# Optimization experiments

Measured on AMD Instinct MI355X. Metric: run time of the kernel, lower is better.

The kernel has to match this reference:

```python
import jax, jax.numpy as jnp
import numpy as np

N, E, C_IN, C_OUT, HEADS = 50000, 800000, 256, 64, 4

def setup_inputs() -> dict:
    key = jax.random.key(0)
    ks = jax.random.split(key, 6)
    x = jax.random.normal(ks[0], (N, C_IN), dtype=jnp.float32)
    row = jax.random.randint(ks[1], (E,), 0, N, dtype=jnp.int32)
    col = jax.random.randint(ks[2], (E,), 0, N, dtype=jnp.int32)
    # ensure no self loops (remove_self_loops is then a no-op)
    col = jnp.where(col == row, (col + 1) % N, col)
    edge_index = jnp.stack([row, col], axis=0)
    edge_attr = jax.random.normal(ks[3], (E,), dtype=jnp.float32)
    weight = jax.random.normal(ks[4], (C_IN, C_OUT), dtype=jnp.float32) * (1.0 / np.sqrt(C_IN))
    kw, kb = jax.random.split(ks[5])
    att_w = jax.random.normal(kw, (2 * C_OUT, HEADS), dtype=jnp.float32) * (1.0 / np.sqrt(2 * C_OUT))
    att_b = jax.random.normal(kb, (HEADS,), dtype=jnp.float32) * 0.01
    return {"x": x, "edge_index": edge_index, "edge_attr": edge_attr,
            "weight": weight, "att_w": att_w, "att_b": att_b}

def _egat_forward(x, edge_index, edge_attr, weight, att_w, att_b):
    n = x.shape[0]
    xp = x @ weight  # [N, C_OUT]
    # add self loops (edge_attr fill value = 1)
    loop = jnp.arange(n, dtype=edge_index.dtype)
    row = jnp.concatenate([edge_index[0], loop])
    col = jnp.concatenate([edge_index[1], loop])
    ea = jnp.concatenate([edge_attr, jnp.ones((n,), dtype=edge_attr.dtype)])
    # per-edge attention logits [E+N, HEADS]
    alpha = jnp.concatenate([xp[row], xp[col]], axis=-1) @ att_w + att_b
    alpha = alpha * jnp.abs(ea)[:, None]
    alpha = jax.nn.leaky_relu(alpha, negative_slope=0.2) * 100.0
    # segment softmax grouped by row
    amax = jax.ops.segment_max(alpha, row, num_segments=n)
    ex = jnp.exp(alpha - amax[row])
    denom = jax.ops.segment_sum(ex, row, num_segments=n)
    alpha = ex / (denom[row] + 1e-16)
    # concat=False -> average heads into a single column
    alpha = alpha.mean(-1)[:, None]  # [E+N, 1]
    # my_cast: [E+N, C_OUT, n_cols]
    out = xp[col][:, :, None] * alpha[:, None, :]
    out = jax.ops.segment_sum(out, row, num_segments=n)  # [N, C_OUT, 1]
    alpha_index = jnp.stack([row, col], axis=0)
    return out, alpha, alpha_index

def reference(x, edge_index, edge_attr, weight, att_w, att_b):
    return _egat_forward(x, edge_index, edge_attr, weight, att_w, att_b)
```

## Files before the change

### kernel.cpp

```cpp
#include <hip/hip_runtime.h>
#include <hip/hip_bf16.h>

#define NN 50000
#define NE 800000
#define MT (NN + NE)
#define CO 64

#define OFF_ALPHA (NN * CO)
#define OFF_IDX   (OFF_ALPHA + MT)

#define WS_XPB  0
#define WS_A1   (WS_XPB + NN * CO / 2)
#define WS_A2   (WS_A1 + NN * 4)
#define WS_CNT  (WS_A2 + NN * 4)
#define WS_SLOT 2050000
#define WS_NEED4 ((size_t)14850000 * 4)

#define GEMM_BLOCKS ((NN + 63) / 64)
#define HIST_BLOCKS ((MT + 255) / 256)

template <bool S4>
__global__ __launch_bounds__(256) void k_gemm_hist(const float* __restrict__ x,
                                                   const float* __restrict__ w,
                                                   __hip_bfloat16* __restrict__ xpb,
                                                   const float* __restrict__ attw,
                                                   float* __restrict__ a1,
                                                   float* __restrict__ a2,
                                                   const int* __restrict__ ei0,
                                                   const int* __restrict__ ei1,
                                                   const float* __restrict__ ea,
                                                   int* __restrict__ cnt,
                                                   int* __restrict__ slot1,
                                                   int4* __restrict__ slot4,
                                                   float* __restrict__ dout) {
  if (blockIdx.x < GEMM_BLOCKS) {
    __shared__ float xs[32][68];
    __shared__ float wsm[32][68];
    const int tid = threadIdx.x;
    const int nb = blockIdx.x * 64;
    const int tr = tid >> 4;
    const int tc = tid & 15;
    const int xn0 = tid >> 3, xq0 = tid & 7;
    const int xn1 = (256 + tid) >> 3, xq1 = tid & 7;
    const int wk0 = tid >> 4, wc0 = tid & 15;
    const int wk1 = (256 + tid) >> 4, wc1 = tid & 15;
    float acc[4][4] = {};
    float4 xv0, xv1, wv0, wv1;

    {
      int gn0 = nb + xn0, gn1 = nb + xn1;
      xv0 = (gn0 < NN) ? *reinterpret_cast<const float4*>(&x[gn0 * 256 + xq0 * 4])
                       : make_float4(0.f, 0.f, 0.f, 0.f);
      xv1 = (gn1 < NN) ? *reinterpret_cast<const float4*>(&x[gn1 * 256 + xq1 * 4])
                       : make_float4(0.f, 0.f, 0.f, 0.f);
      wv0 = *reinterpret_cast<const float4*>(&w[wk0 * CO + wc0 * 4]);
      wv1 = *reinterpret_cast<const float4*>(&w[wk1 * CO + wc1 * 4]);
    }

    for (int kb = 0; kb < 256; kb += 32) {
      xs[xq0 * 4 + 0][xn0] = xv0.x; xs[xq0 * 4 + 1][xn0] = xv0.y;
      xs[xq0 * 4 + 2][xn0] = xv0.z; xs[xq0 * 4 + 3][xn0] = xv0.w;
      xs[xq1 * 4 + 0][xn1] = xv1.x; xs[xq1 * 4 + 1][xn1] = xv1.y;
      xs[xq1 * 4 + 2][xn1] = xv1.z; xs[xq1 * 4 + 3][xn1] = xv1.w;
      *reinterpret_cast<float4*>(&wsm[wk0][wc0 * 4]) = wv0;
      *reinterpret_cast<float4*>(&wsm[wk1][wc1 * 4]) = wv1;
      __syncthreads();
      if (kb < 224) {
        const int nkb = kb + 32;
        int gn0 = nb + xn0, gn1 = nb + xn1;
        xv0 = (gn0 < NN) ? *reinterpret_cast<const float4*>(&x[gn0 * 256 + nkb + xq0 * 4])
                         : make_float4(0.f, 0.f, 0.f, 0.f);
        xv1 = (gn1 < NN) ? *reinterpret_cast<const float4*>(&x[gn1 * 256 + nkb + xq1 * 4])
                         : make_float4(0.f, 0.f, 0.f, 0.f);
        wv0 = *reinterpret_cast<const float4*>(&w[(nkb + wk0) * CO + wc0 * 4]);
        wv1 = *reinterpret_cast<const float4*>(&w[(nkb + wk1) * CO + wc1 * 4]);
      }
#pragma unroll
      for (int kk = 0; kk < 32; ++kk) {
        const float4 xv4 = *reinterpret_cast<const float4*>(&xs[kk][tr * 4]);
        const float4 wv4 = *reinterpret_cast<const float4*>(&wsm[kk][tc * 4]);
        const float xvv[4] = {xv4.x, xv4.y, xv4.z, xv4.w};
        const float wvv[4] = {wv4.x, wv4.y, wv4.z, wv4.w};
#pragma unroll
        for (int i = 0; i < 4; ++i)
#pragma unroll
          for (int j = 0; j < 4; ++j) acc[i][j] = fmaf(xvv[i], wvv[j], acc[i][j]);
      }
      __syncthreads();
    }
#pragma unroll
    for (int i = 0; i < 4; ++i) {
      int gn = nb + tr * 4 + i;
      if (gn < NN) {
        union { ushort4 u4; __hip_bfloat16 h[4]; } pk;
        pk.h[0] = __float2bfloat16(acc[i][0]);
        pk.h[1] = __float2bfloat16(acc[i][1]);
        pk.h[2] = __float2bfloat16(acc[i][2]);
        pk.h[3] = __float2bfloat16(acc[i][3]);
        *reinterpret_cast<ushort4*>(&xpb[gn * CO + tc * 4]) = pk.u4;
      }
    }
    float p1[4][4] = {}, p2[4][4] = {};
#pragma unroll
    for (int j = 0; j < 4; ++j) {
      const float4 w1 = *reinterpret_cast<const float4*>(&attw[(4 * tc + j) * 4]);
      const float4 w2 = *reinterpret_cast<const float4*>(&attw[(64 + 4 * tc + j) * 4]);
#pragma unroll
      for (int i = 0; i < 4; ++i) {
        const float a = acc[i][j];
        p1[i][0] = fmaf(a, w1.x, p1[i][0]); p1[i][1] = fmaf(a, w1.y, p1[i][1]);
        p1[i][2] = fmaf(a, w1.z, p1[i][2]); p1[i][3] = fmaf(a, w1.w, p1[i][3]);
        p2[i][0] = fmaf(a, w2.x, p2[i][0]); p2[i][1] = fmaf(a, w2.y, p2[i][1]);
        p2[i][2] = fmaf(a, w2.z, p2[i][2]); p2[i][3] = fmaf(a, w2.w, p2[i][3]);
      }
    }
#pragma unroll
    for (int off = 1; off < 16; off <<= 1)
#pragma unroll
      for (int i = 0; i < 4; ++i)
#pragma unroll
        for (int h = 0; h < 4; ++h) {
          p1[i][h] += __shfl_xor(p1[i][h], off);
          p2[i][h] += __shfl_xor(p2[i][h], off);
        }
    if (tc == 0) {
#pragma unroll
      for (int i = 0; i < 4; ++i) {
        int gn = nb + tr * 4 + i;
        if (gn < NN) {
          *reinterpret_cast<float4*>(&a1[gn * 4]) =
              make_float4(p1[i][0], p1[i][1], p1[i][2], p1[i][3]);
          *reinterpret_cast<float4*>(&a2[gn * 4]) =
              make_float4(p2[i][0], p2[i][1], p2[i][2], p2[i][3]);
        }
      }
    }
  } else {
    int e = (blockIdx.x - GEMM_BLOCKS) * 256 + threadIdx.x;
    if (e >= MT) return;
    int r, c; float aw;
    if (e < NE) { r = ei0[e]; c = ei1[e]; aw = fabsf(ea[e]); }
    else        { r = e - NE; c = r;      aw = 1.0f; }
    int pos = atomicAdd(&cnt[r], 1);
    if (pos < 64) {
      if (S4) slot4[r * 64 + pos] = make_int4(e, c, __float_as_int(aw), 0);
      else    slot1[r * 64 + pos] = e;
    }
    dout[OFF_IDX + e] = (float)r;
    dout[OFF_IDX + MT + e] = (float)c;
  }
}

template <bool S4>
__global__ __launch_bounds__(256) void k_node(const int* __restrict__ ei1,
                                              const float* __restrict__ ea,
                                              const float* __restrict__ attb,
                                              const __hip_bfloat16* __restrict__ xpb,
                                              const float* __restrict__ a1,
                                              const float* __restrict__ a2,
                                              const int* __restrict__ cnt,
                                              const int* __restrict__ slot1,
                                              const int4* __restrict__ slot4,
                                              float* __restrict__ dout) {
  const int lane = threadIdx.x & 63;
  const int wid = threadIdx.x >> 6;
  const int r = blockIdx.x * 4 + wid;
  if (r >= NN) return;
  const int deg = min(cnt[r], 64);
  const float4 a1r = *reinterpret_cast<const float4*>(&a1[r * 4]);
  const float4 bb = *reinterpret_cast<const float4*>(&attb[0]);

  const bool act = lane < deg;
  int e = 0, c = 0;
  float aw = 0.f;
  if (act) {
    if (S4) {
      int4 sv = slot4[r * 64 + lane];
      e = sv.x; c = sv.y; aw = __int_as_float(sv.z);
    } else {
      e = slot1[r * 64 + lane];
      if (e < NE) { c = ei1[e]; aw = fabsf(ea[e]); }
      else        { c = r;      aw = 1.0f; }
    }
  }
  const float4 a2c = *reinterpret_cast<const float4*>(&a2[c * 4]);
  float t0 = -1e30f, t1 = -1e30f, t2 = -1e30f, t3 = -1e30f;
  if (act) {
    t0 = (a1r.x + a2c.x + bb.x) * aw;
    t1 = (a1r.y + a2c.y + bb.y) * aw;
    t2 = (a1r.z + a2c.z + bb.z) * aw;
    t3 = (a1r.w + a2c.w + bb.w) * aw;
    t0 = (t0 < 0.f ? 0.2f * t0 : t0) * 100.f;
    t1 = (t1 < 0.f ? 0.2f * t1 : t1) * 100.f;
    t2 = (t2 < 0.f ? 0.2f * t2 : t2) * 100.f;
    t3 = (t3 < 0.f ? 0.2f * t3 : t3) * 100.f;
  }
  float m0 = t0, m1 = t1, m2 = t2, m3 = t3;
  if (deg > 32) {
    m0 = fmaxf(m0, __shfl_xor(m0, 32));
    m1 = fmaxf(m1, __shfl_xor(m1, 32));
    m2 = fmaxf(m2, __shfl_xor(m2, 32));
    m3 = fmaxf(m3, __shfl_xor(m3, 32));
  }
  if (deg > 16) {
    m0 = fmaxf(m0, __shfl_xor(m0, 16));
    m1 = fmaxf(m1, __shfl_xor(m1, 16));
    m2 = fmaxf(m2, __shfl_xor(m2, 16));
    m3 = fmaxf(m3, __shfl_xor(m3, 16));
  }
#pragma unroll
  for (int off = 8; off >= 1; off >>= 1) {
    m0 = fmaxf(m0, __shfl_xor(m0, off));
    m1 = fmaxf(m1, __shfl_xor(m1, off));
    m2 = fmaxf(m2, __shfl_xor(m2, off));
    m3 = fmaxf(m3, __shfl_xor(m3, off));
  }
  float p0 = act ? __expf(t0 - m0) : 0.f;
  float p1 = act ? __expf(t1 - m1) : 0.f;
  float p2 = act ? __expf(t2 - m2) : 0.f;
  float p3 = act ? __expf(t3 - m3) : 0.f;
  float s0 = p0, s1 = p1, s2 = p2, s3 = p3;
  if (deg > 32) {
    s0 += __shfl_xor(s0, 32); s1 += __shfl_xor(s1, 32);
    s2 += __shfl_xor(s2, 32); s3 += __shfl_xor(s3, 32);
  }
  if (deg > 16) {
    s0 += __shfl_xor(s0, 16); s1 += __shfl_xor(s1, 16);
    s2 += __shfl_xor(s2, 16); s3 += __shfl_xor(s3, 16);
  }
#pragma unroll
  for (int off = 8; off >= 1; off >>= 1) {
    s0 += __shfl_xor(s0, off); s1 += __shfl_xor(s1, off);
    s2 += __shfl_xor(s2, off); s3 += __shfl_xor(s3, off);
  }
  float mean = 0.f;
  if (act) {
    mean = 0.25f * (p0 / (s0 + 1e-16f) + p1 / (s1 + 1e-16f) +
                    p2 / (s2 + 1e-16f) + p3 / (s3 + 1e-16f));
    dout[OFF_ALPHA + e] = mean;
  }
  const int eg = lane >> 4;
  const int cg = lane & 15;
  float4 acc = make_float4(0.f, 0.f, 0.f, 0.f);
  const int nIter = (deg + 3) >> 2;
  for (int it = 0; it < nIter; ++it) {
    int idx = it * 4 + eg;
    float am = __shfl(mean, idx);
    int cc = __shfl(c, idx);
    ushort4 xv = *reinterpret_cast<const ushort4*>(&xpb[cc * CO + cg * 4]);
    acc.x = fmaf(am, __uint_as_float((unsigned)xv.x << 16), acc.x);
    acc.y = fmaf(am, __uint_as_float((unsigned)xv.y << 16), acc.y);
    acc.z = fmaf(am, __uint_as_float((unsigned)xv.z << 16), acc.z);
    acc.w = fmaf(am, __uint_as_float((unsigned)xv.w << 16), acc.w);
  }
#pragma unroll
  for (int off = 16; off <= 32; off <<= 1) {
    acc.x += __shfl_xor(acc.x, off);
    acc.y += __shfl_xor(acc.y, off);
    acc.z += __shfl_xor(acc.z, off);
    acc.w += __shfl_xor(acc.w, off);
  }
  if (lane < 16) *reinterpret_cast<float4*>(&dout[r * CO + lane * 4]) = acc;
}

extern "C" void kernel_launch(void* const* d_in, const int* in_sizes, int n_in,
                              void* d_out, int out_size, void* d_ws, size_t ws_size,
                              hipStream_t stream) {
  const float* x    = (const float*)d_in[0];
  const int*   ei   = (const int*)d_in[1];
  const float* ea   = (const float*)d_in[2];
  const float* w    = (const float*)d_in[3];
  const float* attw = (const float*)d_in[4];
  const float* attb = (const float*)d_in[5];
  float* dout = (float*)d_out;

  float* wsf = (float*)d_ws;
  __hip_bfloat16* xpb = (__hip_bfloat16*)(wsf + WS_XPB);
  float* a1   = wsf + WS_A1;
  float* a2   = wsf + WS_A2;
  int*   cnt  = (int*)(wsf + WS_CNT);
  int*   slot1 = (int*)(wsf + WS_SLOT);
  int4*  slot4 = (int4*)(wsf + WS_SLOT);
  const int* ei0 = ei;
  const int* ei1 = ei + NE;

  hipMemsetAsync(cnt, 0, NN * sizeof(int), stream);

  const bool use4 = ws_size >= WS_NEED4;
  if (use4) {
    k_gemm_hist<true><<<GEMM_BLOCKS + HIST_BLOCKS, 256, 0, stream>>>(
        x, w, xpb, attw, a1, a2, ei0, ei1, ea, cnt, slot1, slot4, dout);
    k_node<true><<<(NN + 3) / 4, 256, 0, stream>>>(
        ei1, ea, attb, xpb, a1, a2, cnt, slot1, slot4, dout);
  } else {
    k_gemm_hist<false><<<GEMM_BLOCKS + HIST_BLOCKS, 256, 0, stream>>>(
        x, w, xpb, attw, a1, a2, ei0, ei1, ea, cnt, slot1, slot4, dout);
    k_node<false><<<(NN + 3) / 4, 256, 0, stream>>>(
        ei1, ea, attb, xpb, a1, a2, cnt, slot1, slot4, dout);
  }
}
```

Measured before the change: 94.93 us.

## Split fused gemm/histogram kernel and pack edge slots into 8 bytes

The combined GEMM+histogram kernel becomes two launches: a 1024-thread histogram kernel and a separate GEMM kernel. Each slot entry shrinks from an int4 to an int2 by bit-packing the edge id (20 bits), column (16 bits) and a truncated |edge_attr| whose low mantissa bits are dropped. This halves slot write and read traffic and removes the fallback path that re-gathered ei1 and ea. The cost is an extra launch, no more overlap between the GEMM and the histogram, and a small precision loss in the edge weight. The packing relies on N < 65536 and E+N < 2^20.

```diff
diff --git a/kernel.cpp b/kernel.cpp
--- a/kernel.cpp
+++ b/kernel.cpp
@@ -14,153 +14,147 @@
 #define WS_A2   (WS_A1 + NN * 4)
 #define WS_CNT  (WS_A2 + NN * 4)
 #define WS_SLOT 2050000
-#define WS_NEED4 ((size_t)14850000 * 4)
 
 #define GEMM_BLOCKS ((NN + 63) / 64)
-#define HIST_BLOCKS ((MT + 255) / 256)
-
-template <bool S4>
-__global__ __launch_bounds__(256) void k_gemm_hist(const float* __restrict__ x,
-                                                   const float* __restrict__ w,
-                                                   __hip_bfloat16* __restrict__ xpb,
-                                                   const float* __restrict__ attw,
-                                                   float* __restrict__ a1,
-                                                   float* __restrict__ a2,
-                                                   const int* __restrict__ ei0,
-                                                   const int* __restrict__ ei1,
-                                                   const float* __restrict__ ea,
-                                                   int* __restrict__ cnt,
-                                                   int* __restrict__ slot1,
-                                                   int4* __restrict__ slot4,
-                                                   float* __restrict__ dout) {
-  if (blockIdx.x < GEMM_BLOCKS) {
-    __shared__ float xs[32][68];
-    __shared__ float wsm[32][68];
-    const int tid = threadIdx.x;
-    const int nb = blockIdx.x * 64;
-    const int tr = tid >> 4;
-    const int tc = tid & 15;
-    const int xn0 = tid >> 3, xq0 = tid & 7;
-    const int xn1 = (256 + tid) >> 3, xq1 = tid & 7;
-    const int wk0 = tid >> 4, wc0 = tid & 15;
-    const int wk1 = (256 + tid) >> 4, wc1 = tid & 15;
-    float acc[4][4] = {};
-    float4 xv0, xv1, wv0, wv1;
-
-    {
+
+__global__ __launch_bounds__(256) void k_gemm(const float* __restrict__ x,
+                                              const float* __restrict__ w,
+                                              __hip_bfloat16* __restrict__ xpb,
+                                              const float* __restrict__ attw,
+                                              float* __restrict__ a1,
+                                              float* __restrict__ a2) {
+  __shared__ float xs[32][68];
+  __shared__ float wsm[32][68];
+  const int tid = threadIdx.x;
+  const int nb = blockIdx.x * 64;
+  const int tr = tid >> 4;
+  const int tc = tid & 15;
+  const int xn0 = tid >> 3, xq0 = tid & 7;
+  const int xn1 = (256 + tid) >> 3, xq1 = tid & 7;
+  const int wk0 = tid >> 4, wc0 = tid & 15;
+  const int wk1 = (256 + tid) >> 4, wc1 = tid & 15;
+  float acc[4][4] = {};
+  float4 xv0, xv1, wv0, wv1;
+
+  {
+    int gn0 = nb + xn0, gn1 = nb + xn1;
+    xv0 = (gn0 < NN) ? *reinterpret_cast<const float4*>(&x[gn0 * 256 + xq0 * 4])
+                     : make_float4(0.f, 0.f, 0.f, 0.f);
+    xv1 = (gn1 < NN) ? *reinterpret_cast<const float4*>(&x[gn1 * 256 + xq1 * 4])
+                     : make_float4(0.f, 0.f, 0.f, 0.f);
+    wv0 = *reinterpret_cast<const float4*>(&w[wk0 * CO + wc0 * 4]);
+    wv1 = *reinterpret_cast<const float4*>(&w[wk1 * CO + wc1 * 4]);
+  }
+
+  for (int kb = 0; kb < 256; kb += 32) {
+    xs[xq0 * 4 + 0][xn0] = xv0.x; xs[xq0 * 4 + 1][xn0] = xv0.y;
+    xs[xq0 * 4 + 2][xn0] = xv0.z; xs[xq0 * 4 + 3][xn0] = xv0.w;
+    xs[xq1 * 4 + 0][xn1] = xv1.x; xs[xq1 * 4 + 1][xn1] = xv1.y;
+    xs[xq1 * 4 + 2][xn1] = xv1.z; xs[xq1 * 4 + 3][xn1] = xv1.w;
+    *reinterpret_cast<float4*>(&wsm[wk0][wc0 * 4]) = wv0;
+    *reinterpret_cast<float4*>(&wsm[wk1][wc1 * 4]) = wv1;
+    __syncthreads();
+    if (kb < 224) {
+      const int nkb = kb + 32;
       int gn0 = nb + xn0, gn1 = nb + xn1;
-      xv0 = (gn0 < NN) ? *reinterpret_cast<const float4*>(&x[gn0 * 256 + xq0 * 4])
+      xv0 = (gn0 < NN) ? *reinterpret_cast<const float4*>(&x[gn0 * 256 + nkb + xq0 * 4])
                        : make_float4(0.f, 0.f, 0.f, 0.f);
-      xv1 = (gn1 < NN) ? *reinterpret_cast<const float4*>(&x[gn1 * 256 + xq1 * 4])
+      xv1 = (gn1 < NN) ? *reinterpret_cast<const float4*>(&x[gn1 * 256 + nkb + xq1 * 4])
                        : make_float4(0.f, 0.f, 0.f, 0.f);
-      wv0 = *reinterpret_cast<const float4*>(&w[wk0 * CO + wc0 * 4]);
-      wv1 = *reinterpret_cast<const float4*>(&w[wk1 * CO + wc1 * 4]);
-    }
-
-    for (int kb = 0; kb < 256; kb += 32) {
-      xs[xq0 * 4 + 0][xn0] = xv0.x; xs[xq0 * 4 + 1][xn0] = xv0.y;
-      xs[xq0 * 4 + 2][xn0] = xv0.z; xs[xq0 * 4 + 3][xn0] = xv0.w;
-      xs[xq1 * 4 + 0][xn1] = xv1.x; xs[xq1 * 4 + 1][xn1] = xv1.y;
-      xs[xq1 * 4 + 2][xn1] = xv1.z; xs[xq1 * 4 + 3][xn1] = xv1.w;
-      *reinterpret_cast<float4*>(&wsm[wk0][wc0 * 4]) = wv0;
-      *reinterpret_cast<float4*>(&wsm[wk1][wc1 * 4]) = wv1;
-      __syncthreads();
-      if (kb < 224) {
-        const int nkb = kb + 32;
-        int gn0 = nb + xn0, gn1 = nb + xn1;
-        xv0 = (gn0 < NN) ? *reinterpret_cast<const float4*>(&x[gn0 * 256 + nkb + xq0 * 4])
-                         : make_float4(0.f, 0.f, 0.f, 0.f);
-        xv1 = (gn1 < NN) ? *reinterpret_cast<const float4*>(&x[gn1 * 256 + nkb + xq1 * 4])
-                         : make_float4(0.f, 0.f, 0.f, 0.f);
-        wv0 = *reinterpret_cast<const float4*>(&w[(nkb + wk0) * CO + wc0 * 4]);
-        wv1 = *reinterpret_cast<const float4*>(&w[(nkb + wk1) * CO + wc1 * 4]);
+      wv0 = *reinterpret_cast<const float4*>(&w[(nkb + wk0) * CO + wc0 * 4]);
+      wv1 = *reinterpret_cast<const float4*>(&w[(nkb + wk1) * CO + wc1 * 4]);
+    }
+#pragma unroll
+    for (int kk = 0; kk < 32; ++kk) {
+      const float4 xv4 = *reinterpret_cast<const float4*>(&xs[kk][tr * 4]);
+      const float4 wv4 = *reinterpret_cast<const float4*>(&wsm[kk][tc * 4]);
+      const float xvv[4] = {xv4.x, xv4.y, xv4.z, xv4.w};
+      const float wvv[4] = {wv4.x, wv4.y, wv4.z, wv4.w};
+#pragma unroll
+      for (int i = 0; i < 4; ++i)
+#pragma unroll
+        for (int j = 0; j < 4; ++j) acc[i][j] = fmaf(xvv[i], wvv[j], acc[i][j]);
+    }
+    __syncthreads();
+  }
+#pragma unroll
+  for (int i = 0; i < 4; ++i) {
+    int gn = nb + tr * 4 + i;
+    if (gn < NN) {
+      union { ushort4 u4; __hip_bfloat16 h[4]; } pk;
+      pk.h[0] = __float2bfloat16(acc[i][0]);
+      pk.h[1] = __float2bfloat16(acc[i][1]);
+      pk.h[2] = __float2bfloat16(acc[i][2]);
+      pk.h[3] = __float2bfloat16(acc[i][3]);
+      *reinterpret_cast<ushort4*>(&xpb[gn * CO + tc * 4]) = pk.u4;
+    }
+  }
+  float p1[4][4] = {}, p2[4][4] = {};
+#pragma unroll
+  for (int j = 0; j < 4; ++j) {
+    const float4 w1 = *reinterpret_cast<const float4*>(&attw[(4 * tc + j) * 4]);
+    const float4 w2 = *reinterpret_cast<const float4*>(&attw[(64 + 4 * tc + j) * 4]);
+#pragma unroll
+    for (int i = 0; i < 4; ++i) {
+      const float a = acc[i][j];
+      p1[i][0] = fmaf(a, w1.x, p1[i][0]); p1[i][1] = fmaf(a, w1.y, p1[i][1]);
+      p1[i][2] = fmaf(a, w1.z, p1[i][2]); p1[i][3] = fmaf(a, w1.w, p1[i][3]);
+      p2[i][0] = fmaf(a, w2.x, p2[i][0]); p2[i][1] = fmaf(a, w2.y, p2[i][1]);
+      p2[i][2] = fmaf(a, w2.z, p2[i][2]); p2[i][3] = fmaf(a, w2.w, p2[i][3]);
+    }
+  }
+#pragma unroll
+  for (int off = 1; off < 16; off <<= 1)
+#pragma unroll
+    for (int i = 0; i < 4; ++i)
+#pragma unroll
+      for (int h = 0; h < 4; ++h) {
+        p1[i][h] += __shfl_xor(p1[i][h], off);
+        p2[i][h] += __shfl_xor(p2[i][h], off);
       }
-#pragma unroll
-      for (int kk = 0; kk < 32; ++kk) {
-        const float4 xv4 = *reinterpret_cast<const float4*>(&xs[kk][tr * 4]);
-        const float4 wv4 = *reinterpret_cast<const float4*>(&wsm[kk][tc * 4]);
-        const float xvv[4] = {xv4.x, xv4.y, xv4.z, xv4.w};
-        const float wvv[4] = {wv4.x, wv4.y, wv4.z, wv4.w};
-#pragma unroll
-        for (int i = 0; i < 4; ++i)
-#pragma unroll
-          for (int j = 0; j < 4; ++j) acc[i][j] = fmaf(xvv[i], wvv[j], acc[i][j]);
-      }
-      __syncthreads();
-    }
+  if (tc == 0) {
 #pragma unroll
     for (int i = 0; i < 4; ++i) {
       int gn = nb + tr * 4 + i;
       if (gn < NN) {
-        union { ushort4 u4; __hip_bfloat16 h[4]; } pk;
-        pk.h[0] = __float2bfloat16(acc[i][0]);
-        pk.h[1] = __float2bfloat16(acc[i][1]);
-        pk.h[2] = __float2bfloat16(acc[i][2]);
-        pk.h[3] = __float2bfloat16(acc[i][3]);
-        *reinterpret_cast<ushort4*>(&xpb[gn * CO + tc * 4]) = pk.u4;
+        *reinterpret_cast<float4*>(&a1[gn * 4]) =
+            make_float4(p1[i][0], p1[i][1], p1[i][2], p1[i][3]);
+        *reinterpret_cast<float4*>(&a2[gn * 4]) =
+            make_float4(p2[i][0], p2[i][1], p2[i][2], p2[i][3]);
       }
     }
-    float p1[4][4] = {}, p2[4][4] = {};
-#pragma unroll
-    for (int j = 0; j < 4; ++j) {
-      const float4 w1 = *reinterpret_cast<const float4*>(&attw[(4 * tc + j) * 4]);
-      const float4 w2 = *reinterpret_cast<const float4*>(&attw[(64 + 4 * tc + j) * 4]);
-#pragma unroll
-      for (int i = 0; i < 4; ++i) {
-        const float a = acc[i][j];
-        p1[i][0] = fmaf(a, w1.x, p1[i][0]); p1[i][1] = fmaf(a, w1.y, p1[i][1]);
-        p1[i][2] = fmaf(a, w1.z, p1[i][2]); p1[i][3] = fmaf(a, w1.w, p1[i][3]);
-        p2[i][0] = fmaf(a, w2.x, p2[i][0]); p2[i][1] = fmaf(a, w2.y, p2[i][1]);
-        p2[i][2] = fmaf(a, w2.z, p2[i][2]); p2[i][3] = fmaf(a, w2.w, p2[i][3]);
-      }
-    }
-#pragma unroll
-    for (int off = 1; off < 16; off <<= 1)
-#pragma unroll
-      for (int i = 0; i < 4; ++i)
-#pragma unroll
-        for (int h = 0; h < 4; ++h) {
-          p1[i][h] += __shfl_xor(p1[i][h], off);
-          p2[i][h] += __shfl_xor(p2[i][h], off);
-        }
-    if (tc == 0) {
-#pragma unroll
-      for (int i = 0; i < 4; ++i) {
-        int gn = nb + tr * 4 + i;
-        if (gn < NN) {
-          *reinterpret_cast<float4*>(&a1[gn * 4]) =
-              make_float4(p1[i][0], p1[i][1], p1[i][2], p1[i][3]);
-          *reinterpret_cast<float4*>(&a2[gn * 4]) =
-              make_float4(p2[i][0], p2[i][1], p2[i][2], p2[i][3]);
-        }
-      }
-    }
-  } else {
-    int e = (blockIdx.x - GEMM_BLOCKS) * 256 + threadIdx.x;
-    if (e >= MT) return;
-    int r, c; float aw;
-    if (e < NE) { r = ei0[e]; c = ei1[e]; aw = fabsf(ea[e]); }
-    else        { r = e - NE; c = r;      aw = 1.0f; }
-    int pos = atomicAdd(&cnt[r], 1);
-    if (pos < 64) {
-      if (S4) slot4[r * 64 + pos] = make_int4(e, c, __float_as_int(aw), 0);
-      else    slot1[r * 64 + pos] = e;
-    }
-    dout[OFF_IDX + e] = (float)r;
-    dout[OFF_IDX + MT + e] = (float)c;
-  }
-}
-
-template <bool S4>
-__global__ __launch_bounds__(256) void k_node(const int* __restrict__ ei1,
-                                              const float* __restrict__ ea,
-                                              const float* __restrict__ attb,
+  }
+}
+
+__global__ __launch_bounds__(1024) void k_hist(const int* __restrict__ ei0,
+                                               const int* __restrict__ ei1,
+                                               const float* __restrict__ ea,
+                                               int* __restrict__ cnt,
+                                               int2* __restrict__ slot,
+                                               float* __restrict__ dout) {
+  int e = blockIdx.x * 1024 + threadIdx.x;
+  if (e >= MT) return;
+  int r, c; float aw;
+  if (e < NE) { r = ei0[e]; c = ei1[e]; aw = fabsf(ea[e]); }
+  else        { r = e - NE; c = r;      aw = 1.0f; }
+  int pos = atomicAdd(&cnt[r], 1);
+  if (pos < 64) {
+    unsigned awb = __float_as_uint(aw);
+    int2 pk;
+    pk.x = (int)((awb & 0xFFFFFFF0u) | ((unsigned)e >> 16));
+    pk.y = (int)(((unsigned)e & 0xFFFFu) | ((unsigned)c << 16));
+    slot[r * 64 + pos] = pk;
+  }
+  dout[OFF_IDX + e] = (float)r;
+  dout[OFF_IDX + MT + e] = (float)c;
+}
+
+__global__ __launch_bounds__(256) void k_node(const float* __restrict__ attb,
                                               const __hip_bfloat16* __restrict__ xpb,
                                               const float* __restrict__ a1,
                                               const float* __restrict__ a2,
                                               const int* __restrict__ cnt,
-                                              const int* __restrict__ slot1,
-                                              const int4* __restrict__ slot4,
+                                              const int2* __restrict__ slot,
                                               float* __restrict__ dout) {
   const int lane = threadIdx.x & 63;
   const int wid = threadIdx.x >> 6;
@@ -174,14 +168,11 @@
   int e = 0, c = 0;
   float aw = 0.f;
   if (act) {
-    if (S4) {
-      int4 sv = slot4[r * 64 + lane];
-      e = sv.x; c = sv.y; aw = __int_as_float(sv.z);
-    } else {
-      e = slot1[r * 64 + lane];
-      if (e < NE) { c = ei1[e]; aw = fabsf(ea[e]); }
-      else        { c = r;      aw = 1.0f; }
-    }
+    int2 sv = slot[r * 64 + lane];
+    unsigned w0 = (unsigned)sv.x, w1 = (unsigned)sv.y;
+    aw = __uint_as_float(w0 & 0xFFFFFFF0u);
+    e  = (int)(((w0 & 0xFu) << 16) | (w1 & 0xFFFFu));
+    c  = (int)(w1 >> 16);
   }
   const float4 a2c = *reinterpret_cast<const float4*>(&a2[c * 4]);
   float t0 = -1e30f, t1 = -1e30f, t2 = -1e30f, t3 = -1e30f;
@@ -279,23 +270,13 @@
   float* a1   = wsf + WS_A1;
   float* a2   = wsf + WS_A2;
   int*   cnt  = (int*)(wsf + WS_CNT);
-  int*   slot1 = (int*)(wsf + WS_SLOT);
-  int4*  slot4 = (int4*)(wsf + WS_SLOT);
+  int2*  slot = (int2*)(wsf + WS_SLOT);
   const int* ei0 = ei;
   const int* ei1 = ei + NE;
 
   hipMemsetAsync(cnt, 0, NN * sizeof(int), stream);
 
-  const bool use4 = ws_size >= WS_NEED4;
-  if (use4) {
-    k_gemm_hist<true><<<GEMM_BLOCKS + HIST_BLOCKS, 256, 0, stream>>>(
-        x, w, xpb, attw, a1, a2, ei0, ei1, ea, cnt, slot1, slot4, dout);
-    k_node<true><<<(NN + 3) / 4, 256, 0, stream>>>(
-        ei1, ea, attb, xpb, a1, a2, cnt, slot1, slot4, dout);
-  } else {
-    k_gemm_hist<false><<<GEMM_BLOCKS + HIST_BLOCKS, 256, 0, stream>>>(
-        x, w, xpb, attw, a1, a2, ei0, ei1, ea, cnt, slot1, slot4, dout);
-    k_node<false><<<(NN + 3) / 4, 256, 0, stream>>>(
-        ei1, ea, attb, xpb, a1, a2, cnt, slot1, slot4, dout);
-  }
-}
+  k_hist<<<(MT + 1023) / 1024, 1024, 0, stream>>>(ei0, ei1, ea, cnt, slot, dout);
+  k_gemm<<<GEMM_BLOCKS, 256, 0, stream>>>(x, w, xpb, attw, a1, a2);
+  k_node<<<(NN + 3) / 4, 256, 0, stream>>>(attb, xpb, a1, a2, cnt, slot, dout);
+}
```

New measurement: 134.1 us. 1.41x slower.
